# Kernel optimization log

Hardware: AMD Instinct MI355X
Metric: run time of the kernel (lower is better)

## Reference

```python
import jax, jax.numpy as jnp
import numpy as np

N_NODES = 100000


def _gcn_layer(h_in, W, b, src, dst, n_nodes):
    """PyG GCNConv: out = D^{-1/2} (A + I) D^{-1/2} (h_in @ W) + b.
    src/dst already include self-loops. Messages flow src -> dst."""
    h = h_in @ W  # [N, C_out]
    ones = jnp.ones(dst.shape[0], dtype=h.dtype)
    deg = jax.ops.segment_sum(ones, dst, num_segments=n_nodes)  # in-degree incl. self-loops
    dinv = jnp.where(deg > 0, jax.lax.rsqrt(deg), 0.0)
    norm = dinv[src] * dinv[dst]  # [E]
    msg = norm[:, None] * h[src]  # gather + scale, [E, C_out]
    out = jax.ops.segment_sum(msg, dst, num_segments=n_nodes)
    return out + b


def setup_inputs() -> dict:
    key = jax.random.key(0)
    ks = jax.random.split(key, 4)
    d_in, d_hid = 64, 64
    n_edges = 1600000
    x = jax.random.normal(ks[0], (N_NODES, d_in), dtype=jnp.float32)
    edge_index = jax.random.randint(ks[1], (2, n_edges), 0, N_NODES, dtype=jnp.int64)
    W1 = jax.random.normal(ks[2], (d_in, d_hid), dtype=jnp.float32) * (1.0 / np.sqrt(d_in))
    b1 = jnp.zeros((d_hid,), dtype=jnp.float32)
    W2 = jax.random.normal(ks[3], (d_hid, d_hid), dtype=jnp.float32) * (1.0 / np.sqrt(d_hid))
    b2 = jnp.zeros((d_hid,), dtype=jnp.float32)
    return {"x": x, "edge_index": edge_index, "W1": W1, "b1": b1, "W2": W2, "b2": b2}


def reference(x, edge_index, W1, b1, W2, b2):
    n = x.shape[0]
    loop = jnp.arange(n, dtype=edge_index.dtype)
    src = jnp.concatenate([edge_index[0], loop])  # add self-loops once, reused by both layers
    dst = jnp.concatenate([edge_index[1], loop])
    h = jax.nn.relu(_gcn_layer(x, W1, b1, src, dst, n))
    h = jax.nn.relu(_gcn_layer(h, W2, b2, src, dst, n))
    return h
```

## Files before the change

kernel.cpp:

```cpp
#include <hip/hip_runtime.h>
#include <hip/hip_bf16.h>


#define NDIM 64
#define BSHIFT 9
#define BNODES (1 << BSHIFT)
#define BCAP 10240
#define CHUNK 4096
#define STAGE_CAP 16384

typedef __attribute__((ext_vector_type(8))) short short8b;
typedef __attribute__((ext_vector_type(4))) float f32x4;

__device__ __forceinline__ unsigned f2bf_rne(float f) {
  unsigned u = __float_as_uint(f);
  return (u + 0x7fffu + ((u >> 16) & 1u)) >> 16;
}

__global__ void init_cursor_kernel(int* __restrict__ bcursor, int nbuck) {
  int b = blockIdx.x * 256 + threadIdx.x;
  if (b < nbuck) bcursor[b] = b * BCAP;
}

__global__ __launch_bounds__(256) void bin_scatter_kernel(
    const int* __restrict__ src, const int* __restrict__ dst,
    int* __restrict__ bcursor, unsigned* __restrict__ binned, int nedges) {
  __shared__ int lcnt[256], lbase[256], lcur[256], gbase[256], tscan[256];
  __shared__ int2 stage[CHUNK];
  int t = threadIdx.x;
  int i0 = blockIdx.x * CHUNK;
  int iend = i0 + CHUNK; if (iend > nedges) iend = nedges;
  lcnt[t] = 0;
  __syncthreads();
  for (int i = i0 + t; i < iend; i += 256)
    atomicAdd(&lcnt[dst[i] >> BSHIFT], 1);
  __syncthreads();
  tscan[t] = lcnt[t];
  __syncthreads();
  for (int off = 1; off < 256; off <<= 1) {
    int tv = (t >= off) ? tscan[t - off] : 0;
    __syncthreads();
    tscan[t] += tv;
    __syncthreads();
  }
  lbase[t] = tscan[t] - lcnt[t];
  lcur[t] = lbase[t];
  if (lcnt[t] > 0) gbase[t] = atomicAdd(&bcursor[t], lcnt[t]);
  __syncthreads();
  for (int i = i0 + t; i < iend; i += 256) {
    int s = src[i], d = dst[i];
    int p = atomicAdd(&lcur[d >> BSHIFT], 1);
    stage[p] = make_int2(s, d);
  }
  __syncthreads();
  int cnt = iend - i0;
  for (int i = t; i < cnt; i += 256) {
    int2 pr = stage[i];
    int b = pr.y >> BSHIFT;
    unsigned pk = (((unsigned)(pr.y & (BNODES - 1))) << 17) | (unsigned)pr.x;
    int idx = gbase[b] + (i - lbase[b]);
    if (idx < (b + 1) * BCAP) binned[idx] = pk;
  }
}

__global__ __launch_bounds__(256) void csr_build_kernel(
    const unsigned* __restrict__ binned, const int* __restrict__ bcursor,
    int* __restrict__ rowbeg, int* __restrict__ rowend,
    int* __restrict__ csr_src, float* __restrict__ dinv, int n) {
  __shared__ int deg[BNODES], rpl[BNODES], cur[BNODES], tscan[256];
  __shared__ int stage[STAGE_CAP];
  int b = blockIdx.x, t = threadIdx.x;
  int node0 = b << BSHIFT;
  int ncnt = n - node0; if (ncnt > BNODES) ncnt = BNODES;
  int e0 = b * BCAP;
  int ecnt = bcursor[b] - e0;
  deg[t] = 0; deg[t + 256] = 0;
  __syncthreads();
  for (int i = t; i < ecnt; i += 256)
    atomicAdd(&deg[binned[e0 + i] >> 17], 1);
  __syncthreads();
  int d0 = deg[2 * t], d1 = deg[2 * t + 1];
  int ps = d0 + d1;
  tscan[t] = ps;
  __syncthreads();
  for (int off = 1; off < 256; off <<= 1) {
    int tv = (t >= off) ? tscan[t - off] : 0;
    __syncthreads();
    tscan[t] += tv;
    __syncthreads();
  }
  int eb = tscan[t] - ps;
  rpl[2 * t] = eb;          cur[2 * t] = eb;
  rpl[2 * t + 1] = eb + d0; cur[2 * t + 1] = eb + d0;
  __syncthreads();
  for (int i = t; i < ncnt; i += 256) {
    rowbeg[node0 + i] = e0 + rpl[i];
    rowend[node0 + i] = e0 + rpl[i] + deg[i];
    dinv[node0 + i] = rsqrtf((float)deg[i] + 1.0f);
  }
  bool fit = ecnt <= STAGE_CAP;
  for (int i = t; i < ecnt; i += 256) {
    unsigned pk = binned[e0 + i];
    int p = atomicAdd(&cur[pk >> 17], 1);
    int s = (int)(pk & 0x1FFFFu);
    if (fit) stage[p] = s;
    else csr_src[e0 + p] = s;
  }
  __syncthreads();
  if (fit) {
    for (int i = t; i < ecnt; i += 256) csr_src[e0 + i] = stage[i];
  }
}

template <bool BF16IN>
__global__ __launch_bounds__(256) void gemm_mfma_kernel(
    const void* __restrict__ Xin, const float* __restrict__ W,
    const float* __restrict__ dinv, ushort* __restrict__ hsb, int nrows) {
  __shared__ __attribute__((aligned(16))) ushort stage[4][16 * NDIM];
  const int tid = threadIdx.x;
  const int l = tid & 63;
  const int wv = tid >> 6;
  const int lrow = l & 15;
  const int kg = l >> 4;

  short8b Whi[4][2], Wlo[4][2];
#pragma unroll
  for (int ct = 0; ct < 4; ++ct) {
#pragma unroll
    for (int ks = 0; ks < 2; ++ks) {
      const int c = ct * 16 + lrow;
      const int k0 = ks * 32 + kg * 8;
#pragma unroll
      for (int i = 0; i < 8; ++i) {
        float w = W[(k0 + i) * NDIM + c];
        unsigned hb = f2bf_rne(w);
        float hf = __uint_as_float(hb << 16);
        Whi[ct][ks][i] = (short)hb;
        Wlo[ct][ks][i] = (short)f2bf_rne(w - hf);
      }
    }
  }

  const int tiles = (nrows + 15) >> 4;
  for (int tb = blockIdx.x * 4; tb < tiles; tb += gridDim.x * 4) {
    const int t = tb + wv;
    const int row0 = t << 4;
    const int r = row0 + lrow;
    short8b Ahi[2], Alo[2];
    if (BF16IN) {
      const uint4* Xb = (const uint4*)Xin;
#pragma unroll
      for (int ks = 0; ks < 2; ++ks) {
        uint4 q = make_uint4(0u, 0u, 0u, 0u);
        if (r < nrows) q = Xb[(size_t)r * 8 + ks * 4 + kg];
        union { uint4 u; short8b s; } cv; cv.u = q;
        Ahi[ks] = cv.s;
        Alo[ks] = cv.s;
      }
    } else {
      const float4* Xf = (const float4*)Xin;
#pragma unroll
      for (int ks = 0; ks < 2; ++ks) {
        float4 xa = make_float4(0.f, 0.f, 0.f, 0.f);
        float4 xb = make_float4(0.f, 0.f, 0.f, 0.f);
        if (r < nrows) {
          xa = Xf[(size_t)r * 16 + ks * 8 + kg * 2];
          xb = Xf[(size_t)r * 16 + ks * 8 + kg * 2 + 1];
        }
        float xs[8] = {xa.x, xa.y, xa.z, xa.w, xb.x, xb.y, xb.z, xb.w};
#pragma unroll
        for (int i = 0; i < 8; ++i) {
          unsigned hb = f2bf_rne(xs[i]);
          float hf = __uint_as_float(hb << 16);
          Ahi[ks][i] = (short)hb;
          Alo[ks][i] = (short)f2bf_rne(xs[i] - hf);
        }
      }
    }
    f32x4 acc[4];
#pragma unroll
    for (int ct = 0; ct < 4; ++ct) {
      f32x4 a = {0.f, 0.f, 0.f, 0.f};
#pragma unroll
      for (int ks = 0; ks < 2; ++ks) {
        a = __builtin_amdgcn_mfma_f32_16x16x32_bf16(Ahi[ks], Whi[ct][ks], a, 0, 0, 0);
        a = __builtin_amdgcn_mfma_f32_16x16x32_bf16(Ahi[ks], Wlo[ct][ks], a, 0, 0, 0);
        if (!BF16IN)
          a = __builtin_amdgcn_mfma_f32_16x16x32_bf16(Alo[ks], Whi[ct][ks], a, 0, 0, 0);
      }
      acc[ct] = a;
    }
#pragma unroll
    for (int q = 0; q < 4; ++q) {
      const int rr = row0 + kg * 4 + q;
      const float di = (rr < nrows) ? dinv[rr] : 0.f;
#pragma unroll
      for (int ct = 0; ct < 4; ++ct)
        stage[wv][(kg * 4 + q) * NDIM + ct * 16 + lrow] =
            (ushort)f2bf_rne(acc[ct][q] * di);
    }
    __syncthreads();
#pragma unroll
    for (int e = 0; e < 2; ++e) {
      const int idx = e * 64 + l;
      const int rw = idx >> 3;
      if (row0 + rw < nrows)
        ((uint4*)hsb)[(size_t)(row0 + rw) * 8 + (idx & 7)] =
            ((const uint4*)stage[wv])[idx];
    }
    __syncthreads();
  }
}

template <bool BF16OUT>
__global__ __launch_bounds__(256) void agg_epi_kernel(
    const int* __restrict__ rowbeg, const int* __restrict__ rowend,
    const int* __restrict__ csr_src, const ushort* __restrict__ hsb,
    const float* __restrict__ dinv, const float* __restrict__ bias,
    void* __restrict__ outp, int n) {
  const int node = blockIdx.x * 4 + (threadIdx.x >> 6);
  if (node >= n) return;
  const int l = threadIdx.x & 63;
  const int beg = rowbeg[node], end = rowend[node];
  float acc0 = __uint_as_float((unsigned)hsb[(size_t)node * NDIM + l] << 16);
  float acc1 = 0.f;
  for (int base = beg; base < end; base += 64) {
    int m = end - base; if (m > 64) m = 64;
    int sidx = (l < m) ? csr_src[base + l] : 0;
    int j = 0;
    for (; j + 8 <= m; j += 8) {
      int s0 = __builtin_amdgcn_readlane(sidx, j + 0);
      int s1 = __builtin_amdgcn_readlane(sidx, j + 1);
      int s2 = __builtin_amdgcn_readlane(sidx, j + 2);
      int s3 = __builtin_amdgcn_readlane(sidx, j + 3);
      int s4 = __builtin_amdgcn_readlane(sidx, j + 4);
      int s5 = __builtin_amdgcn_readlane(sidx, j + 5);
      int s6 = __builtin_amdgcn_readlane(sidx, j + 6);
      int s7 = __builtin_amdgcn_readlane(sidx, j + 7);
      ushort u0 = hsb[(size_t)s0 * NDIM + l];
      ushort u1 = hsb[(size_t)s1 * NDIM + l];
      ushort u2 = hsb[(size_t)s2 * NDIM + l];
      ushort u3 = hsb[(size_t)s3 * NDIM + l];
      ushort u4 = hsb[(size_t)s4 * NDIM + l];
      ushort u5 = hsb[(size_t)s5 * NDIM + l];
      ushort u6 = hsb[(size_t)s6 * NDIM + l];
      ushort u7 = hsb[(size_t)s7 * NDIM + l];
      acc0 += __uint_as_float((unsigned)u0 << 16);
      acc1 += __uint_as_float((unsigned)u1 << 16);
      acc0 += __uint_as_float((unsigned)u2 << 16);
      acc1 += __uint_as_float((unsigned)u3 << 16);
      acc0 += __uint_as_float((unsigned)u4 << 16);
      acc1 += __uint_as_float((unsigned)u5 << 16);
      acc0 += __uint_as_float((unsigned)u6 << 16);
      acc1 += __uint_as_float((unsigned)u7 << 16);
    }
#pragma unroll
    for (int e = 0; e < 7; ++e) {
      if (j + e < m) {
        int s = __builtin_amdgcn_readlane(sidx, j + e);
        acc0 += __uint_as_float((unsigned)hsb[(size_t)s * NDIM + l] << 16);
      }
    }
  }
  float o = fmaxf(fmaf(dinv[node], acc0 + acc1, bias[l]), 0.f);
  if (BF16OUT)
    ((ushort*)outp)[(size_t)node * NDIM + l] = (ushort)f2bf_rne(o);
  else
    ((float*)outp)[(size_t)node * NDIM + l] = o;
}

extern "C" void kernel_launch(void* const* d_in, const int* in_sizes, int n_in,
                              void* d_out, int out_size, void* d_ws, size_t ws_size,
                              hipStream_t stream) {
  const float* x  = (const float*)d_in[0];
  const int* eidx = (const int*)d_in[1];
  const float* W1 = (const float*)d_in[2];
  const float* b1 = (const float*)d_in[3];
  const float* W2 = (const float*)d_in[4];
  const float* b2 = (const float*)d_in[5];
  float* out = (float*)d_out;

  const int N = in_sizes[0] / NDIM;
  const int E = in_sizes[1] / 2;
  const int* src = eidx;
  const int* dst = eidx + E;
  const int NV = N * NDIM;
  const int nbuck = (N + BNODES - 1) >> BSHIFT;
  const int nchunk = (E + CHUNK - 1) / CHUNK;

  char* w = (char*)d_ws;
  unsigned* binned = (unsigned*)w;  w += (size_t)nbuck * BCAP * 4;
  int*   csr_src = (int*)w;    w += (size_t)nbuck * BCAP * 4;
  int*   rowbeg  = (int*)w;    w += ((size_t)(N + 4) & ~3ull) * 4;
  int*   rowend  = (int*)w;    w += ((size_t)(N + 4) & ~3ull) * 4;
  float* dinv    = (float*)w;  w += ((size_t)(N + 4) & ~3ull) * 4;
  int*   bcursor = (int*)w;    w += 512 * 4;
  ushort* hsb = (ushort*)w;  w += (size_t)NV * 2;
  ushort* h2b = (ushort*)w;

  init_cursor_kernel<<<1, 256, 0, stream>>>(bcursor, nbuck);
  bin_scatter_kernel<<<nchunk, 256, 0, stream>>>(src, dst, bcursor, binned, E);
  csr_build_kernel<<<nbuck, 256, 0, stream>>>(binned, bcursor, rowbeg, rowend,
                                              csr_src, dinv, N);

  gemm_mfma_kernel<false><<<512, 256, 0, stream>>>(x, W1, dinv, hsb, N);
  agg_epi_kernel<true><<<(N + 3) / 4, 256, 0, stream>>>(
      rowbeg, rowend, csr_src, hsb, dinv, b1, h2b, N);

  gemm_mfma_kernel<true><<<512, 256, 0, stream>>>(h2b, W2, dinv, hsb, N);
  agg_epi_kernel<false><<<(N + 3) / 4, 256, 0, stream>>>(
      rowbeg, rowend, csr_src, hsb, dinv, b2, out, N);
}
```

Baseline: 265.6 us.

## Vectorize gather with 16-byte loads per 8-lane subgroup and sort CSR by source phase

The aggregation kernel now splits each wavefront into 8 subgroups. Each lane loads a uint4 holding 8 bf16 features, so one wave gathers 8 neighbor rows per instruction instead of one 2-byte element per lane, and the partial sums are combined with xor-shuffles at the end. The CSR build replaces its LDS staging buffer with per-node, per-source-range counters, so neighbor lists come out roughly sorted by source index, which is meant to improve gather locality in L2. Workspace buffers are also aligned to 128 bytes. In exchange the epilogue gains a shuffle reduction, and the CSR scatter now writes straight to global memory instead of through LDS.

```diff
diff --git a/kernel.cpp b/kernel.cpp
--- a/kernel.cpp
+++ b/kernel.cpp
@@ -7,8 +7,10 @@
 #define BNODES (1 << BSHIFT)
 #define BCAP 10240
 #define CHUNK 4096
-#define STAGE_CAP 16384
-
+#define PHASES 13
+#define PSHIFT 13
+
+typedef float v2f __attribute__((ext_vector_type(2)));
 typedef __attribute__((ext_vector_type(8))) short short8b;
 typedef __attribute__((ext_vector_type(4))) float f32x4;
 
@@ -67,17 +69,31 @@
     const unsigned* __restrict__ binned, const int* __restrict__ bcursor,
     int* __restrict__ rowbeg, int* __restrict__ rowend,
     int* __restrict__ csr_src, float* __restrict__ dinv, int n) {
-  __shared__ int deg[BNODES], rpl[BNODES], cur[BNODES], tscan[256];
-  __shared__ int stage[STAGE_CAP];
+  __shared__ int deg[BNODES], rpl[BNODES], tscan[256];
+  __shared__ int pcnt[BNODES * PHASES];
   int b = blockIdx.x, t = threadIdx.x;
   int node0 = b << BSHIFT;
   int ncnt = n - node0; if (ncnt > BNODES) ncnt = BNODES;
   int e0 = b * BCAP;
   int ecnt = bcursor[b] - e0;
-  deg[t] = 0; deg[t + 256] = 0;
-  __syncthreads();
-  for (int i = t; i < ecnt; i += 256)
-    atomicAdd(&deg[binned[e0 + i] >> 17], 1);
+  if (ecnt > BCAP) ecnt = BCAP;
+  for (int i = t; i < BNODES * PHASES; i += 256) pcnt[i] = 0;
+  __syncthreads();
+  for (int i = t; i < ecnt; i += 256) {
+    unsigned u = binned[e0 + i];
+    atomicAdd(&pcnt[(u >> 17) * PHASES + ((u & 0x1FFFFu) >> PSHIFT)], 1);
+  }
+  __syncthreads();
+  for (int i = t; i < BNODES; i += 256) {
+    int s = 0;
+#pragma unroll
+    for (int p = 0; p < PHASES; ++p) {
+      int c = pcnt[i * PHASES + p];
+      pcnt[i * PHASES + p] = s;
+      s += c;
+    }
+    deg[i] = s;
+  }
   __syncthreads();
   int d0 = deg[2 * t], d1 = deg[2 * t + 1];
   int ps = d0 + d1;
@@ -90,25 +106,21 @@
     __syncthreads();
   }
   int eb = tscan[t] - ps;
-  rpl[2 * t] = eb;          cur[2 * t] = eb;
-  rpl[2 * t + 1] = eb + d0; cur[2 * t + 1] = eb + d0;
+  rpl[2 * t] = eb;
+  rpl[2 * t + 1] = eb + d0;
   __syncthreads();
   for (int i = t; i < ncnt; i += 256) {
     rowbeg[node0 + i] = e0 + rpl[i];
     rowend[node0 + i] = e0 + rpl[i] + deg[i];
     dinv[node0 + i] = rsqrtf((float)deg[i] + 1.0f);
   }
-  bool fit = ecnt <= STAGE_CAP;
+  __syncthreads();
   for (int i = t; i < ecnt; i += 256) {
-    unsigned pk = binned[e0 + i];
-    int p = atomicAdd(&cur[pk >> 17], 1);
-    int s = (int)(pk & 0x1FFFFu);
-    if (fit) stage[p] = s;
-    else csr_src[e0 + p] = s;
-  }
-  __syncthreads();
-  if (fit) {
-    for (int i = t; i < ecnt; i += 256) csr_src[e0 + i] = stage[i];
+    unsigned u = binned[e0 + i];
+    int nd = u >> 17;
+    int s = (int)(u & 0x1FFFFu);
+    int pos = rpl[nd] + atomicAdd(&pcnt[nd * PHASES + (s >> PSHIFT)], 1);
+    csr_src[e0 + pos] = s;
   }
 }
 
@@ -212,61 +224,84 @@
   }
 }
 
+__device__ __forceinline__ void add8(v2f* acc, uint4 q) {
+  v2f a0, a1, a2, a3;
+  a0.x = __uint_as_float(q.x << 16); a0.y = __uint_as_float(q.x & 0xffff0000u);
+  a1.x = __uint_as_float(q.y << 16); a1.y = __uint_as_float(q.y & 0xffff0000u);
+  a2.x = __uint_as_float(q.z << 16); a2.y = __uint_as_float(q.z & 0xffff0000u);
+  a3.x = __uint_as_float(q.w << 16); a3.y = __uint_as_float(q.w & 0xffff0000u);
+  acc[0] += a0; acc[1] += a1; acc[2] += a2; acc[3] += a3;
+}
+
 template <bool BF16OUT>
 __global__ __launch_bounds__(256) void agg_epi_kernel(
     const int* __restrict__ rowbeg, const int* __restrict__ rowend,
-    const int* __restrict__ csr_src, const ushort* __restrict__ hsb,
-    const float* __restrict__ dinv, const float* __restrict__ bias,
+    const int* __restrict__ csr_src, const uint4* __restrict__ hsb4,
+    const float* __restrict__ dinv, const float4* __restrict__ b4,
     void* __restrict__ outp, int n) {
-  const int node = blockIdx.x * 4 + (threadIdx.x >> 6);
+  int node = blockIdx.x * 4 + (threadIdx.x >> 6);
   if (node >= n) return;
-  const int l = threadIdx.x & 63;
-  const int beg = rowbeg[node], end = rowend[node];
-  float acc0 = __uint_as_float((unsigned)hsb[(size_t)node * NDIM + l] << 16);
-  float acc1 = 0.f;
+  int l = threadIdx.x & 63;
+  int sub = l >> 3, g = l & 7;
+  int beg = rowbeg[node], end = rowend[node];
+  v2f acc[4];
+#pragma unroll
+  for (int i = 0; i < 4; ++i) acc[i] = (v2f)(0.f);
   for (int base = beg; base < end; base += 64) {
     int m = end - base; if (m > 64) m = 64;
     int sidx = (l < m) ? csr_src[base + l] : 0;
     int j = 0;
-    for (; j + 8 <= m; j += 8) {
-      int s0 = __builtin_amdgcn_readlane(sidx, j + 0);
-      int s1 = __builtin_amdgcn_readlane(sidx, j + 1);
-      int s2 = __builtin_amdgcn_readlane(sidx, j + 2);
-      int s3 = __builtin_amdgcn_readlane(sidx, j + 3);
-      int s4 = __builtin_amdgcn_readlane(sidx, j + 4);
-      int s5 = __builtin_amdgcn_readlane(sidx, j + 5);
-      int s6 = __builtin_amdgcn_readlane(sidx, j + 6);
-      int s7 = __builtin_amdgcn_readlane(sidx, j + 7);
-      ushort u0 = hsb[(size_t)s0 * NDIM + l];
-      ushort u1 = hsb[(size_t)s1 * NDIM + l];
-      ushort u2 = hsb[(size_t)s2 * NDIM + l];
-      ushort u3 = hsb[(size_t)s3 * NDIM + l];
-      ushort u4 = hsb[(size_t)s4 * NDIM + l];
-      ushort u5 = hsb[(size_t)s5 * NDIM + l];
-      ushort u6 = hsb[(size_t)s6 * NDIM + l];
-      ushort u7 = hsb[(size_t)s7 * NDIM + l];
-      acc0 += __uint_as_float((unsigned)u0 << 16);
-      acc1 += __uint_as_float((unsigned)u1 << 16);
-      acc0 += __uint_as_float((unsigned)u2 << 16);
-      acc1 += __uint_as_float((unsigned)u3 << 16);
-      acc0 += __uint_as_float((unsigned)u4 << 16);
-      acc1 += __uint_as_float((unsigned)u5 << 16);
-      acc0 += __uint_as_float((unsigned)u6 << 16);
-      acc1 += __uint_as_float((unsigned)u7 << 16);
-    }
-#pragma unroll
-    for (int e = 0; e < 7; ++e) {
-      if (j + e < m) {
-        int s = __builtin_amdgcn_readlane(sidx, j + e);
-        acc0 += __uint_as_float((unsigned)hsb[(size_t)s * NDIM + l] << 16);
-      }
-    }
-  }
-  float o = fmaxf(fmaf(dinv[node], acc0 + acc1, bias[l]), 0.f);
-  if (BF16OUT)
-    ((ushort*)outp)[(size_t)node * NDIM + l] = (ushort)f2bf_rne(o);
-  else
-    ((float*)outp)[(size_t)node * NDIM + l] = o;
+    for (; j + 16 <= m; j += 16) {
+      int s0 = __shfl(sidx, j + sub);
+      int s1 = __shfl(sidx, j + 8 + sub);
+      uint4 q0 = hsb4[(size_t)s0 * 8 + g];
+      uint4 q1 = hsb4[(size_t)s1 * 8 + g];
+      add8(acc, q0);
+      add8(acc, q1);
+    }
+    for (; j < m; j += 8) {
+      int e = j + sub;
+      int s = __shfl(sidx, e < m ? e : 0);
+      uint4 q = hsb4[(size_t)s * 8 + g];
+      if (e < m) add8(acc, q);
+    }
+  }
+  if (sub == 0) add8(acc, hsb4[(size_t)node * 8 + g]);
+  float a[8];
+#pragma unroll
+  for (int i = 0; i < 4; ++i) { a[2 * i] = acc[i].x; a[2 * i + 1] = acc[i].y; }
+#pragma unroll
+  for (int i = 0; i < 8; ++i) {
+    a[i] += __shfl_xor(a[i], 8);
+    a[i] += __shfl_xor(a[i], 16);
+    a[i] += __shfl_xor(a[i], 32);
+  }
+  if (sub == 0) {
+    float di = dinv[node];
+    float4 bb0 = b4[2 * g], bb1 = b4[2 * g + 1];
+    float o[8];
+    o[0] = fmaxf(di * a[0] + bb0.x, 0.f);
+    o[1] = fmaxf(di * a[1] + bb0.y, 0.f);
+    o[2] = fmaxf(di * a[2] + bb0.z, 0.f);
+    o[3] = fmaxf(di * a[3] + bb0.w, 0.f);
+    o[4] = fmaxf(di * a[4] + bb1.x, 0.f);
+    o[5] = fmaxf(di * a[5] + bb1.y, 0.f);
+    o[6] = fmaxf(di * a[6] + bb1.z, 0.f);
+    o[7] = fmaxf(di * a[7] + bb1.w, 0.f);
+    if (BF16OUT) {
+      uint4 wv;
+      wv.x = f2bf_rne(o[0]) | (f2bf_rne(o[1]) << 16);
+      wv.y = f2bf_rne(o[2]) | (f2bf_rne(o[3]) << 16);
+      wv.z = f2bf_rne(o[4]) | (f2bf_rne(o[5]) << 16);
+      wv.w = f2bf_rne(o[6]) | (f2bf_rne(o[7]) << 16);
+      ((uint4*)outp)[(size_t)node * 8 + g] = wv;
+    } else {
+      float4 o0 = make_float4(o[0], o[1], o[2], o[3]);
+      float4 o1 = make_float4(o[4], o[5], o[6], o[7]);
+      ((float4*)outp)[(size_t)node * 16 + 2 * g] = o0;
+      ((float4*)outp)[(size_t)node * 16 + 2 * g + 1] = o1;
+    }
+  }
 }
 
 extern "C" void kernel_launch(void* const* d_in, const int* in_sizes, int n_in,
@@ -288,14 +323,15 @@
   const int nbuck = (N + BNODES - 1) >> BSHIFT;
   const int nchunk = (E + CHUNK - 1) / CHUNK;
 
+  auto al128 = [](size_t v) { return (v + 127) & ~(size_t)127; };
   char* w = (char*)d_ws;
-  unsigned* binned = (unsigned*)w;  w += (size_t)nbuck * BCAP * 4;
-  int*   csr_src = (int*)w;    w += (size_t)nbuck * BCAP * 4;
-  int*   rowbeg  = (int*)w;    w += ((size_t)(N + 4) & ~3ull) * 4;
-  int*   rowend  = (int*)w;    w += ((size_t)(N + 4) & ~3ull) * 4;
-  float* dinv    = (float*)w;  w += ((size_t)(N + 4) & ~3ull) * 4;
-  int*   bcursor = (int*)w;    w += 512 * 4;
-  ushort* hsb = (ushort*)w;  w += (size_t)NV * 2;
+  unsigned* binned = (unsigned*)w;  w += al128((size_t)nbuck * BCAP * 4);
+  int*   csr_src = (int*)w;    w += al128((size_t)nbuck * BCAP * 4);
+  int*   rowbeg  = (int*)w;    w += al128((size_t)N * 4);
+  int*   rowend  = (int*)w;    w += al128((size_t)N * 4);
+  float* dinv    = (float*)w;  w += al128((size_t)N * 4);
+  int*   bcursor = (int*)w;    w += 2048;
+  ushort* hsb = (ushort*)w;  w += al128((size_t)NV * 2);
   ushort* h2b = (ushort*)w;
 
   init_cursor_kernel<<<1, 256, 0, stream>>>(bcursor, nbuck);
@@ -305,9 +341,9 @@
 
   gemm_mfma_kernel<false><<<512, 256, 0, stream>>>(x, W1, dinv, hsb, N);
   agg_epi_kernel<true><<<(N + 3) / 4, 256, 0, stream>>>(
-      rowbeg, rowend, csr_src, hsb, dinv, b1, h2b, N);
+      rowbeg, rowend, csr_src, (const uint4*)hsb, dinv, (const float4*)b1, h2b, N);
 
   gemm_mfma_kernel<true><<<512, 256, 0, stream>>>(h2b, W2, dinv, hsb, N);
   agg_epi_kernel<false><<<(N + 3) / 4, 256, 0, stream>>>(
-      rowbeg, rowend, csr_src, hsb, dinv, b2, out, N);
-}
+      rowbeg, rowend, csr_src, (const uint4*)hsb, dinv, (const float4*)b2, out, N);
+}
```

Result: faster. 245.8 us (-7.4%).
